# Optimization experiments

Measured on AMD Instinct MI355X. Metric: run time of the kernel, lower is better.

Reference implementation:

```python
import jax, jax.numpy as jnp
import numpy as np


def setup_inputs() -> dict:
    key = jax.random.key(0)
    attn = jax.random.uniform(key, (64, 1024, 1024), dtype=jnp.float32)
    return {"attn": attn}


def reference(attn) -> jnp.ndarray:
    # attn: [B, N, N]. For each sample, group strictly-upper-triangular
    # elements by diagonal offset k = j - i (k = 1..N-2; the k = N-1
    # diagonal has a single element and is excluded, matching the torch
    # loop `for i in range(len(distance_record) - 1)`).
    # For offset k: std (unbiased, ddof=1) of diag elements scaled by
    # (N-k)/5, i.e. std(x) * (N-k)/5. Then mean over k, then mean over B.
    B, N = attn.shape[0], attn.shape[1]
    ii = jnp.arange(N)
    off = ii[None, :] - ii[:, None]              # [N, N], j - i
    upper = off >= 1                              # strict upper triangle
    seg = jnp.where(upper, off, 0).reshape(-1)    # segment id per element
    m = upper.reshape(-1).astype(attn.dtype)      # mask lower/diag to 0

    x = attn.reshape(B, -1) * m                   # [B, N*N]
    segsum = lambda v: jax.ops.segment_sum(v, seg, num_segments=N)
    s1 = jax.vmap(segsum)(x)                      # [B, N] per-offset sums
    s2 = jax.vmap(segsum)(x * x)                  # [B, N] per-offset sum sq

    n = (N - jnp.arange(N)).astype(attn.dtype)    # count per offset k
    mean = s1 / n
    denom = jnp.maximum(n - 1.0, 1.0)             # ddof=1; guard k=N-1 (excluded)
    var = jnp.maximum(s2 - n * mean * mean, 0.0) / denom
    std = jnp.sqrt(var) * (n / 5.0)               # std of scaled values

    per_sample = jnp.mean(std[:, 1:N - 1], axis=1)  # offsets 1..N-2
    return jnp.mean(per_sample)
```

## Files before the change

kernel.cpp:

```cpp
#include <hip/hip_runtime.h>


#define NN 1024
#define NB 64
#define WSTRIDE 1032

template<int RCH>
__global__ __launch_bounds__(256) void diag_pass1(
    const float* __restrict__ attn, float* __restrict__ ws) {
  const int b = blockIdx.x / RCH;
  const int c = blockIdx.x % RCH;
  const int t = threadIdx.x;
  int p = (4 - (c & 3)) & 3; if (p == 0) p = 4;

  const float* __restrict__ base = attn + ((size_t)b << 20);
  const int k0 = p + 4 * t;

  float s1x = 0.f, s1y = 0.f, s1z = 0.f, s1w = 0.f;
  float s2x = 0.f, s2y = 0.f, s2z = 0.f, s2w = 0.f;
  float e1 = 0.f, e2 = 0.f;
  const int ek = t - 248;

  #pragma unroll 4
  for (int i = c; i < NN; i += RCH) {
    const int lim = NN - i;
    const float* __restrict__ rowd = base + (size_t)i * (NN + 1);
    if (k0 < lim) {
      const float4 v = *reinterpret_cast<const float4*>(rowd + k0);
      const float x0 = v.x;
      const float x1 = (k0 + 1 < lim) ? v.y : 0.f;
      const float x2 = (k0 + 2 < lim) ? v.z : 0.f;
      const float x3 = (k0 + 3 < lim) ? v.w : 0.f;
      s1x += x0; s2x += x0 * x0;
      s1y += x1; s2y += x1 * x1;
      s1z += x2; s2z += x2 * x2;
      s1w += x3; s2w += x3 * x3;
    }
    if (ek >= 1 && ek < p && ek < lim) {
      const float x = rowd[ek];
      e1 += x; e2 += x * x;
    }
  }

  float* __restrict__ w1 = ws + (size_t)blockIdx.x * (2 * WSTRIDE);
  float* __restrict__ w2 = w1 + WSTRIDE;
  *reinterpret_cast<float4*>(w1 + 4 * t) = make_float4(s1x, s1y, s1z, s1w);
  *reinterpret_cast<float4*>(w2 + 4 * t) = make_float4(s2x, s2y, s2z, s2w);
  if (ek >= 1 && ek < p) {
    w1[1024 + ek] = e1;
    w2[1024 + ek] = e2;
  }
}

template<int RCH>
__global__ __launch_bounds__(256) void diag_pass2(
    const float* __restrict__ ws, float* __restrict__ part) {
  const int b  = blockIdx.x >> 2;
  const int kc = blockIdx.x & 3;
  const int t  = threadIdx.x;
  const int k  = kc * 256 + t;

  float acc = 0.f;
  if (k >= 1 && k <= NN - 2) {
    float s1 = 0.f, s2 = 0.f;
    #pragma unroll
    for (int c = 0; c < RCH; ++c) {
      int p = (4 - (c & 3)) & 3; if (p == 0) p = 4;
      const float* __restrict__ w1 =
          ws + (size_t)(b * RCH + c) * (2 * WSTRIDE);
      const float* __restrict__ w2 = w1 + WSTRIDE;
      const int s = k - p;
      const int idx = (s >= 0) ? s : (1024 + k);
      s1 += w1[idx];
      s2 += w2[idx];
    }
    const float n = (float)(NN - k);
    const float mean = s1 / n;
    const float var = fmaxf(s2 - n * mean * mean, 0.f) / (n - 1.f);
    acc = sqrtf(var) * (n * 0.2f);
  }

  __shared__ float red[256];
  red[t] = acc;
  __syncthreads();
  #pragma unroll
  for (int s = 128; s > 0; s >>= 1) {
    if (t < s) red[t] += red[t + s];
    __syncthreads();
  }
  if (t == 0) part[blockIdx.x] = red[0];
}

__global__ __launch_bounds__(64) void diag_pass3(
    const float* __restrict__ part, float* __restrict__ out) {
  const int t = threadIdx.x;
  float v = part[4 * t] + part[4 * t + 1] + part[4 * t + 2] + part[4 * t + 3];
  v *= (1.0f / 1022.0f);
  #pragma unroll
  for (int s = 32; s > 0; s >>= 1) v += __shfl_down(v, s);
  if (t == 0) out[0] = v * (1.0f / 64.0f);
}

extern "C" void kernel_launch(void* const* d_in, const int* in_sizes, int n_in,
                              void* d_out, int out_size, void* d_ws, size_t ws_size,
                              hipStream_t stream) {
  const float* attn = (const float*)d_in[0];
  float* out = (float*)d_out;
  float* ws = (float*)d_ws;

  const size_t need16 = ((size_t)NB * 16 * 2 * WSTRIDE + NB * 4) * 4;
  const size_t need8  = ((size_t)NB * 8  * 2 * WSTRIDE + NB * 4) * 4;

  if (ws_size >= need16) {
    constexpr int RCH = 16;
    float* part = ws + (size_t)NB * RCH * 2 * WSTRIDE;
    diag_pass1<RCH><<<NB * RCH, 256, 0, stream>>>(attn, ws);
    diag_pass2<RCH><<<NB * 4, 256, 0, stream>>>(ws, part);
    diag_pass3<<<1, 64, 0, stream>>>(part, out);
  } else if (ws_size >= need8) {
    constexpr int RCH = 8;
    float* part = ws + (size_t)NB * RCH * 2 * WSTRIDE;
    diag_pass1<RCH><<<NB * RCH, 256, 0, stream>>>(attn, ws);
    diag_pass2<RCH><<<NB * 4, 256, 0, stream>>>(ws, part);
    diag_pass3<<<1, 64, 0, stream>>>(part, out);
  } else {
    constexpr int RCH = 4;
    float* part = ws + (size_t)NB * RCH * 2 * WSTRIDE;
    diag_pass1<RCH><<<NB * RCH, 256, 0, stream>>>(attn, ws);
    diag_pass2<RCH><<<NB * 4, 256, 0, stream>>>(ws, part);
    diag_pass3<<<1, 64, 0, stream>>>(part, out);
  }
}
```

Before: 43.34 us.

## Unroll diagonal loads with precomputed trip counts and fuse final reduction via atomic counter

```diff
diff --git a/kernel.cpp b/kernel.cpp
--- a/kernel.cpp
+++ b/kernel.cpp
@@ -7,38 +7,80 @@
 
 template<int RCH>
 __global__ __launch_bounds__(256) void diag_pass1(
-    const float* __restrict__ attn, float* __restrict__ ws) {
+    const float* __restrict__ attn, float* __restrict__ ws,
+    unsigned int* __restrict__ counter) {
   const int b = blockIdx.x / RCH;
   const int c = blockIdx.x % RCH;
   const int t = threadIdx.x;
+  if (blockIdx.x == 0 && t == 0)
+    __hip_atomic_store(counter, 0u, __ATOMIC_RELAXED, __HIP_MEMORY_SCOPE_AGENT);
+
   int p = (4 - (c & 3)) & 3; if (p == 0) p = 4;
-
   const float* __restrict__ base = attn + ((size_t)b << 20);
   const int k0 = p + 4 * t;
 
+  int M = (NN - k0 - c + RCH - 1) / RCH;
+  if (M < 0) M = 0;
+
+  const size_t rstride = (size_t)RCH * (NN + 1);
+  const float* ptr = base + (size_t)c * (NN + 1) + k0;
+
   float s1x = 0.f, s1y = 0.f, s1z = 0.f, s1w = 0.f;
   float s2x = 0.f, s2y = 0.f, s2z = 0.f, s2w = 0.f;
+
+  int m = 0;
+  for (; m + 9 <= M; m += 8) {
+    float4 v0 = *reinterpret_cast<const float4*>(ptr + 0 * rstride);
+    float4 v1 = *reinterpret_cast<const float4*>(ptr + 1 * rstride);
+    float4 v2 = *reinterpret_cast<const float4*>(ptr + 2 * rstride);
+    float4 v3 = *reinterpret_cast<const float4*>(ptr + 3 * rstride);
+    float4 v4 = *reinterpret_cast<const float4*>(ptr + 4 * rstride);
+    float4 v5 = *reinterpret_cast<const float4*>(ptr + 5 * rstride);
+    float4 v6 = *reinterpret_cast<const float4*>(ptr + 6 * rstride);
+    float4 v7 = *reinterpret_cast<const float4*>(ptr + 7 * rstride);
+    ptr += 8 * rstride;
+    s1x += v0.x; s2x += v0.x * v0.x; s1y += v0.y; s2y += v0.y * v0.y;
+    s1z += v0.z; s2z += v0.z * v0.z; s1w += v0.w; s2w += v0.w * v0.w;
+    s1x += v1.x; s2x += v1.x * v1.x; s1y += v1.y; s2y += v1.y * v1.y;
+    s1z += v1.z; s2z += v1.z * v1.z; s1w += v1.w; s2w += v1.w * v1.w;
+    s1x += v2.x; s2x += v2.x * v2.x; s1y += v2.y; s2y += v2.y * v2.y;
+    s1z += v2.z; s2z += v2.z * v2.z; s1w += v2.w; s2w += v2.w * v2.w;
+    s1x += v3.x; s2x += v3.x * v3.x; s1y += v3.y; s2y += v3.y * v3.y;
+    s1z += v3.z; s2z += v3.z * v3.z; s1w += v3.w; s2w += v3.w * v3.w;
+    s1x += v4.x; s2x += v4.x * v4.x; s1y += v4.y; s2y += v4.y * v4.y;
+    s1z += v4.z; s2z += v4.z * v4.z; s1w += v4.w; s2w += v4.w * v4.w;
+    s1x += v5.x; s2x += v5.x * v5.x; s1y += v5.y; s2y += v5.y * v5.y;
+    s1z += v5.z; s2z += v5.z * v5.z; s1w += v5.w; s2w += v5.w * v5.w;
+    s1x += v6.x; s2x += v6.x * v6.x; s1y += v6.y; s2y += v6.y * v6.y;
+    s1z += v6.z; s2z += v6.z * v6.z; s1w += v6.w; s2w += v6.w * v6.w;
+    s1x += v7.x; s2x += v7.x * v7.x; s1y += v7.y; s2y += v7.y * v7.y;
+    s1z += v7.z; s2z += v7.z * v7.z; s1w += v7.w; s2w += v7.w * v7.w;
+  }
+  for (; m + 2 <= M; ++m) {
+    float4 v = *reinterpret_cast<const float4*>(ptr);
+    ptr += rstride;
+    s1x += v.x; s2x += v.x * v.x; s1y += v.y; s2y += v.y * v.y;
+    s1z += v.z; s2z += v.z * v.z; s1w += v.w; s2w += v.w * v.w;
+  }
+  if (m < M) {
+    const int lim = NN - (c + RCH * m);
+    float4 v = *reinterpret_cast<const float4*>(ptr);
+    const float x0 = v.x;
+    const float x1 = (k0 + 1 < lim) ? v.y : 0.f;
+    const float x2 = (k0 + 2 < lim) ? v.z : 0.f;
+    const float x3 = (k0 + 3 < lim) ? v.w : 0.f;
+    s1x += x0; s2x += x0 * x0; s1y += x1; s2y += x1 * x1;
+    s1z += x2; s2z += x2 * x2; s1w += x3; s2w += x3 * x3;
+  }
+
+  const int ek = t - 248;
   float e1 = 0.f, e2 = 0.f;
-  const int ek = t - 248;
-
-  #pragma unroll 4
-  for (int i = c; i < NN; i += RCH) {
-    const int lim = NN - i;
-    const float* __restrict__ rowd = base + (size_t)i * (NN + 1);
-    if (k0 < lim) {
-      const float4 v = *reinterpret_cast<const float4*>(rowd + k0);
-      const float x0 = v.x;
-      const float x1 = (k0 + 1 < lim) ? v.y : 0.f;
-      const float x2 = (k0 + 2 < lim) ? v.z : 0.f;
-      const float x3 = (k0 + 3 < lim) ? v.w : 0.f;
-      s1x += x0; s2x += x0 * x0;
-      s1y += x1; s2y += x1 * x1;
-      s1z += x2; s2z += x2 * x2;
-      s1w += x3; s2w += x3 * x3;
-    }
-    if (ek >= 1 && ek < p && ek < lim) {
-      const float x = rowd[ek];
+  if (ek >= 1 && ek < p) {
+    const float* eptr = base + (size_t)c * (NN + 1) + ek;
+    for (int i = c; i < NN - ek; i += RCH) {
+      const float x = *eptr;
       e1 += x; e2 += x * x;
+      eptr += rstride;
     }
   }
 
@@ -54,7 +96,8 @@
 
 template<int RCH>
 __global__ __launch_bounds__(256) void diag_pass2(
-    const float* __restrict__ ws, float* __restrict__ part) {
+    const float* __restrict__ ws, float* __restrict__ part,
+    unsigned int* __restrict__ counter, float* __restrict__ out) {
   const int b  = blockIdx.x >> 2;
   const int kc = blockIdx.x & 3;
   const int t  = threadIdx.x;
@@ -88,17 +131,35 @@
     if (t < s) red[t] += red[t + s];
     __syncthreads();
   }
-  if (t == 0) part[blockIdx.x] = red[0];
+
+  __shared__ unsigned int amLast;
+  if (t == 0) {
+    __hip_atomic_store(&part[blockIdx.x], red[0],
+                       __ATOMIC_RELEASE, __HIP_MEMORY_SCOPE_AGENT);
+    const unsigned int old = __hip_atomic_fetch_add(
+        counter, 1u, __ATOMIC_ACQ_REL, __HIP_MEMORY_SCOPE_AGENT);
+    amLast = (old == gridDim.x - 1) ? 1u : 0u;
+  }
+  __syncthreads();
+  if (amLast && t < 64) {
+    float v = 0.f;
+    #pragma unroll
+    for (int j = 0; j < 4; ++j)
+      v += __hip_atomic_load(&part[4 * t + j],
+                             __ATOMIC_ACQUIRE, __HIP_MEMORY_SCOPE_AGENT);
+    #pragma unroll
+    for (int s = 32; s > 0; s >>= 1) v += __shfl_down(v, s);
+    if (t == 0) out[0] = v * (1.0f / (1022.0f * 64.0f));
+  }
 }
 
-__global__ __launch_bounds__(64) void diag_pass3(
-    const float* __restrict__ part, float* __restrict__ out) {
-  const int t = threadIdx.x;
-  float v = part[4 * t] + part[4 * t + 1] + part[4 * t + 2] + part[4 * t + 3];
-  v *= (1.0f / 1022.0f);
-  #pragma unroll
-  for (int s = 32; s > 0; s >>= 1) v += __shfl_down(v, s);
-  if (t == 0) out[0] = v * (1.0f / 64.0f);
+template<int RCH>
+static void launch_all(const float* attn, float* out, float* ws,
+                       hipStream_t stream) {
+  float* part = ws + (size_t)NB * RCH * 2 * WSTRIDE;
+  unsigned int* counter = (unsigned int*)(part + 256);
+  diag_pass1<RCH><<<NB * RCH, 256, 0, stream>>>(attn, ws, counter);
+  diag_pass2<RCH><<<NB * 4, 256, 0, stream>>>(ws, part, counter, out);
 }
 
 extern "C" void kernel_launch(void* const* d_in, const int* in_sizes, int n_in,
@@ -108,26 +169,10 @@
   float* out = (float*)d_out;
   float* ws = (float*)d_ws;
 
-  const size_t need16 = ((size_t)NB * 16 * 2 * WSTRIDE + NB * 4) * 4;
-  const size_t need8  = ((size_t)NB * 8  * 2 * WSTRIDE + NB * 4) * 4;
+  const size_t need16 = ((size_t)NB * 16 * 2 * WSTRIDE + 256 + 1) * 4;
+  const size_t need8  = ((size_t)NB * 8  * 2 * WSTRIDE + 256 + 1) * 4;
 
-  if (ws_size >= need16) {
-    constexpr int RCH = 16;
-    float* part = ws + (size_t)NB * RCH * 2 * WSTRIDE;
-    diag_pass1<RCH><<<NB * RCH, 256, 0, stream>>>(attn, ws);
-    diag_pass2<RCH><<<NB * 4, 256, 0, stream>>>(ws, part);
-    diag_pass3<<<1, 64, 0, stream>>>(part, out);
-  } else if (ws_size >= need8) {
-    constexpr int RCH = 8;
-    float* part = ws + (size_t)NB * RCH * 2 * WSTRIDE;
-    diag_pass1<RCH><<<NB * RCH, 256, 0, stream>>>(attn, ws);
-    diag_pass2<RCH><<<NB * 4, 256, 0, stream>>>(ws, part);
-    diag_pass3<<<1, 64, 0, stream>>>(part, out);
-  } else {
-    constexpr int RCH = 4;
-    float* part = ws + (size_t)NB * RCH * 2 * WSTRIDE;
-    diag_pass1<RCH><<<NB * RCH, 256, 0, stream>>>(attn, ws);
-    diag_pass2<RCH><<<NB * 4, 256, 0, stream>>>(ws, part);
-    diag_pass3<<<1, 64, 0, stream>>>(part, out);
-  }
+  if (ws_size >= need16)      launch_all<16>(attn, out, ws, stream);
+  else if (ws_size >= need8)  launch_all<8>(attn, out, ws, stream);
+  else                        launch_all<4>(attn, out, ws, stream);
 }
```

Measured after the change: 54.10 us. 24.8% more time.
